# Kernel optimization log

Hardware: AMD Instinct MI355X
Metric: run time of the kernel (lower is better)

Reference implementation:

```python
import jax, jax.numpy as jnp
import numpy as np

S, B, DIN, DBERT, H, L = 128, 32, 256, 768, 512, 2
NT_POS, NT_MORPH = 32, 64


def setup_inputs() -> dict:
    key = jax.random.key(0)
    ks = iter(jax.random.split(key, 32))
    def rn(shape, s=0.1):
        return jax.random.normal(next(ks), shape, dtype=jnp.float32) * s
    D0 = DIN + DBERT  # 1024 == 2*H, so per-layer LSTM weights stack cleanly
    return {
        "src_segments": rn((S, B, DIN), 1.0),
        "bert_encodings": rn((B, DBERT), 1.0),
        "labels_pos": jax.random.randint(next(ks), (S, B), 0, NT_POS, dtype=jnp.int32),
        "labels_morph": jax.random.randint(next(ks), (S, B), 0, NT_MORPH, dtype=jnp.int32),
        # stacked LSTM params: [layer, direction, ...], PyTorch gate order i,f,g,o
        "w_ih": rn((L, 2, 4 * H, D0)),
        "w_hh": rn((L, 2, 4 * H, H)),
        "b_ih": rn((L, 2, 4 * H)),
        "b_hh": rn((L, 2, 4 * H)),
        "head_w_pos": rn((NT_POS, 2 * H)),
        "head_b_pos": rn((NT_POS,)),
        "head_w_morph": rn((NT_MORPH, 2 * H)),
        "head_b_morph": rn((NT_MORPH,)),
        "start_pos": rn((NT_POS,)), "end_pos": rn((NT_POS,)), "trans_pos": rn((NT_POS, NT_POS)),
        "start_morph": rn((NT_MORPH,)), "end_morph": rn((NT_MORPH,)), "trans_morph": rn((NT_MORPH, NT_MORPH)),
    }


def _run_dir(x, w_ih, w_hh, b):
    # x: [S, B, D]; one LSTM direction via scan over time
    bsz, hd = x.shape[1], w_hh.shape[1]
    def step(carry, xt):
        h, c = carry
        g = xt @ w_ih.T + h @ w_hh.T + b  # [B, 4H]
        i, f, gg, o = jnp.split(g, 4, axis=-1)
        c = jax.nn.sigmoid(f) * c + jax.nn.sigmoid(i) * jnp.tanh(gg)
        h = jax.nn.sigmoid(o) * jnp.tanh(c)
        return (h, c), h
    init = (jnp.zeros((bsz, hd), x.dtype), jnp.zeros((bsz, hd), x.dtype))
    _, hs = jax.lax.scan(step, init, x)
    return hs


def _bilstm(x, w_ih, w_hh, b_ih, b_hh):
    out = x
    for l in range(w_ih.shape[0]):
        b = b_ih[l] + b_hh[l]
        fwd = _run_dir(out, w_ih[l, 0], w_hh[l, 0], b[0])
        bwd = _run_dir(out[::-1], w_ih[l, 1], w_hh[l, 1], b[1])[::-1]
        out = jnp.concatenate([fwd, bwd], axis=-1)  # [S, B, 2H]
    return out


def _crf_ll(em, tags, start, trans, end):
    # torchcrf log-likelihood, mask=None, reduction='sum'. em: [S,B,K], tags: [S,B]
    bsz = em.shape[1]
    first = start[tags[0]] + em[0, jnp.arange(bsz), tags[0]]
    em_sc = jnp.take_along_axis(em, tags[..., None], axis=2)[..., 0]  # [S,B]
    num = first + trans[tags[:-1], tags[1:]].sum(0) + em_sc[1:].sum(0) + end[tags[-1]]
    def step(alpha, et):  # alpha: [B,K]
        return jax.nn.logsumexp(alpha[:, :, None] + trans[None], axis=1) + et, None
    alpha, _ = jax.lax.scan(step, start[None, :] + em[0], em[1:])
    den = jax.nn.logsumexp(alpha + end[None, :], axis=1)
    return jnp.sum(num - den)


def reference(src_segments, bert_encodings, labels_pos, labels_morph,
              w_ih, w_hh, b_ih, b_hh,
              head_w_pos, head_b_pos, head_w_morph, head_b_morph,
              start_pos, end_pos, trans_pos, start_morph, end_morph, trans_morph):
    # bert encodings are repeated over seq and concatenated on features
    bert = jnp.broadcast_to(bert_encodings[None], (src_segments.shape[0],) + bert_encodings.shape)
    emb = jnp.concatenate([src_segments, bert], axis=-1)  # dropout p=0 -> identity
    out = _bilstm(emb, w_ih, w_hh, b_ih, b_hh)            # [S,B,2H]
    feat_pos = out @ head_w_pos.T + head_b_pos            # [S,B,32]
    feat_morph = out @ head_w_morph.T + head_b_morph      # [S,B,64]
    ll = (_crf_ll(feat_pos, labels_pos, start_pos, trans_pos, end_pos)
          + _crf_ll(feat_morph, labels_morph, start_morph, trans_morph, end_morph))
    return -ll  # loss = -sum_f crf_f(emissions_f, labels_f)
```

## Files before the change

### kernel.cpp

```cpp
#include <hip/hip_runtime.h>


typedef unsigned short u16;
typedef unsigned int u32;
typedef unsigned long long u64;
typedef __attribute__((ext_vector_type(8))) __bf16 bf16x8;
typedef __attribute__((ext_vector_type(4))) float floatx4;

static __device__ __forceinline__ u16 f2bf(float f) {
  u32 u = __float_as_uint(f);
  u += 0x7fffu + ((u >> 16) & 1u);
  return (u16)(u >> 16);
}
static __device__ __forceinline__ float bf2f(u32 bits) {
  return __uint_as_float(bits << 16);
}
static __device__ __forceinline__ float sigf(float x) {
  return 1.0f / (1.0f + __expf(-x));
}
static __device__ __forceinline__ float tanh_(float x) {
  return 1.0f - 2.0f / (1.0f + __expf(2.0f * x));
}
static __device__ __forceinline__ floatx4 mfma16(bf16x8 a, bf16x8 b, floatx4 c) {
  return __builtin_amdgcn_mfma_f32_16x16x32_bf16(a, b, c, 0, 0, 0);
}

__global__ __launch_bounds__(256) void prep_kernel(
    const float* __restrict__ w_ih, const float* __restrict__ w_hh,
    const float* __restrict__ b_ih, const float* __restrict__ b_hh,
    const float* __restrict__ src,  const float* __restrict__ bert,
    const float* __restrict__ hwp,  const float* __restrict__ hbp,
    const float* __restrict__ hwm,  const float* __restrict__ hbm,
    u16* __restrict__ Wsrc, u16* __restrict__ Wbert, u16* __restrict__ Wih1,
    u16* __restrict__ Whh,  u16* __restrict__ SrcBf, u16* __restrict__ BertBf,
    u16* __restrict__ Wheads, float* __restrict__ b0sum, float* __restrict__ b1sum,
    float* __restrict__ hb, float* __restrict__ dout)
{
  const int NA = 4194304;
  const int NB = 4194304;
  const int NC = 4194304;
  const int ND = 1048576;
  const int NE = 24576;
  const int NF = 98304;
  const int NG = 8192;
  const int NH = 96;
  const int TOTAL = NA + NB + NC + ND + NE + NF + NG + NH + 1;
  for (int i = blockIdx.x * 256 + threadIdx.x; i < TOTAL; i += gridDim.x * 256) {
    int x = i;
    if (x < NA) {
      int c = x & 1023, r = x >> 10;
      float v = w_ih[x];
      if (c < 256) Wsrc[r * 256 + c] = f2bf(v);
      else         Wbert[r * 768 + (c - 256)] = f2bf(v);
      continue;
    }
    x -= NA;
    if (x < NB) { Wih1[x] = f2bf(w_ih[NA + x]); continue; }
    x -= NB;
    if (x < NC) { Whh[x] = f2bf(w_hh[x]); continue; }
    x -= NC;
    if (x < ND) { SrcBf[x] = f2bf(src[x]); continue; }
    x -= ND;
    if (x < NE) { BertBf[x] = f2bf(bert[x]); continue; }
    x -= NE;
    if (x < NF) {
      Wheads[x] = f2bf(x < 32768 ? hwp[x] : hwm[x - 32768]);
      continue;
    }
    x -= NF;
    if (x < NG) {
      float v = b_ih[x] + b_hh[x];
      if (x < 4096) b0sum[x] = v; else b1sum[x - 4096] = v;
      continue;
    }
    x -= NG;
    if (x < NH) { hb[x] = (x < 32) ? hbp[x] : hbm[x - 32]; continue; }
    dout[0] = 0.f;
  }
}

__global__ __launch_bounds__(256) void gemm_nt(
    const u16* __restrict__ A, int lda,
    const u16* __restrict__ B, int ldb,
    float* __restrict__ C, int ldc,
    int M, int N, int K,
    const float* __restrict__ bias_n,
    const float* __restrict__ auxBN, int auxld,
    int mode)
{
  __shared__ __align__(16) u16 As[128 * 64];
  __shared__ __align__(16) u16 Bs[128 * 64];
  const int m0 = blockIdx.y * 128, n0 = blockIdx.x * 128;
  const int tid = threadIdx.x;
  const int wv = tid >> 6, ln = tid & 63;
  const int wm = wv & 1, wn = wv >> 1;
  const int q = ln >> 4, l15 = ln & 15;
  floatx4 acc[4][4];
#pragma unroll
  for (int a = 0; a < 4; ++a)
#pragma unroll
    for (int b2 = 0; b2 < 4; ++b2) acc[a][b2] = (floatx4){0.f, 0.f, 0.f, 0.f};

  for (int kk = 0; kk < K; kk += 64) {
    __syncthreads();
#pragma unroll
    for (int j = 0; j < 4; ++j) {
      const int idx = j * 256 + tid;
      const int r = idx >> 3, cc = idx & 7;
      const int slot = cc ^ (r & 7);
      const int ra = min(m0 + r, M - 1);
      *(int4*)&As[r * 64 + slot * 8] = *(const int4*)&A[(long)ra * lda + kk + cc * 8];
      const int rb = min(n0 + r, N - 1);
      *(int4*)&Bs[r * 64 + slot * 8] = *(const int4*)&B[(long)rb * ldb + kk + cc * 8];
    }
    __syncthreads();
#pragma unroll
    for (int ks = 0; ks < 2; ++ks) {
      bf16x8 af[4], bf[4];
#pragma unroll
      for (int im = 0; im < 4; ++im) {
        const int r = wm * 64 + im * 16 + l15;
        const int slot = (ks * 4 + q) ^ (r & 7);
        af[im] = *(const bf16x8*)&As[r * 64 + slot * 8];
      }
#pragma unroll
      for (int jn = 0; jn < 4; ++jn) {
        const int r = wn * 64 + jn * 16 + l15;
        const int slot = (ks * 4 + q) ^ (r & 7);
        bf[jn] = *(const bf16x8*)&Bs[r * 64 + slot * 8];
      }
#pragma unroll
      for (int im = 0; im < 4; ++im)
#pragma unroll
        for (int jn = 0; jn < 4; ++jn)
          acc[im][jn] = mfma16(af[im], bf[jn], acc[im][jn]);
    }
  }
  if (mode == 0) {
#pragma unroll
    for (int im = 0; im < 4; ++im)
#pragma unroll
      for (int jn = 0; jn < 4; ++jn) {
        const int n = n0 + wn * 64 + jn * 16 + l15;
        if (n < N) {
          const float badd = bias_n ? bias_n[n] : 0.f;
#pragma unroll
          for (int rg = 0; rg < 4; ++rg) {
            const int m = m0 + wm * 64 + im * 16 + q * 4 + rg;
            if (m < M) {
              float v = acc[im][jn][rg] + badd;
              if (auxBN) v += auxBN[(long)(m & 31) * auxld + n];
              C[(long)m * ldc + n] = v;
            }
          }
        }
      }
  } else {
    u64* G = (u64*)C;
#pragma unroll
    for (int im = 0; im < 4; ++im)
#pragma unroll
      for (int jn = 0; jn < 4; ++jn) {
        const int n = n0 + wn * 64 + jn * 16 + l15;
        const int dirsel = n >> 11, nn = n & 2047;
        const int gt = nn >> 9, u = nn & 511;
        const int ub = u >> 4, low = u & 15;
        const int wvl = low >> 2, jl = low & 3;
        const int l15l = gt * 4 + jl;
        const int m = m0 + wm * 64 + im * 16 + q * 4;
        const int s = m >> 5, b0 = m & 31;
        const int mh = b0 >> 4, qq = (b0 >> 2) & 3;
        const float badd = bias_n ? bias_n[n] : 0.f;
        u64 pk = 0;
#pragma unroll
        for (int rg = 0; rg < 4; ++rg) {
          float v = acc[im][jn][rg] + badd;
          if (auxBN) v += auxBN[(long)(b0 + rg) * auxld + n];
          pk |= (u64)f2bf(v) << (16 * rg);
        }
        G[(((((long)dirsel * 128 + s) * 2 + mh) * 32 + ub) * 4 + wvl) * 64
          + l15l * 4 + qq] = pk;
      }
  }
}

__global__ __launch_bounds__(256, 1) void lstm_rec(
    const u16* __restrict__ gates,
    u16* __restrict__ out,
    const u16* __restrict__ whh)
{
  __shared__ __align__(16) u16 h_lds[16 * 512];
  __shared__ float gsc[4][16][17];
  const int bid = blockIdx.x;
  const int dir = bid >> 6;
  const int mh = (bid >> 5) & 1;
  const int ub = bid & 31;
  const int u0 = ub * 16;
  const int tid = threadIdx.x;
  const int wv = tid >> 6;
  const int ln = tid & 63;
  const int q = ln >> 4, l15 = ln & 15;

  const int gate_r = (l15 >> 2) * 512 + u0 + wv * 4 + (l15 & 3);

  bf16x8 bfrag[16];
  {
    const u16* wp = whh + ((long)dir * 2048 + gate_r) * 512 + q * 8;
#pragma unroll
    for (int ks = 0; ks < 16; ++ks)
      bfrag[ks] = *(const bf16x8*)(wp + ks * 32);
  }

  float c = 0.f;
  const int b_glob = mh * 16 + l15;

  const u64* gbase = (const u64*)gates
      + ((((long)dir * 128 * 2 + mh) * 32 + ub) * 4 + wv) * 64 + l15 * 4 + q;

  u64 gcur = gbase[(long)(dir ? 127 : 0) * 16384];
  u64 gnext = 0;

  for (int t = 0; t < 128; ++t) {
    const int s = dir ? (127 - t) : t;
    if (t < 127) {
      const int sn = dir ? (126 - t) : (t + 1);
      gnext = gbase[(long)sn * 16384];
    }
    floatx4 acc = (floatx4){0.f, 0.f, 0.f, 0.f};
    if (t > 0) {
      const int sp = dir ? (s + 1) : (s - 1);
      const u64* ubp = (const u64*)(out + (((long)sp * 32 + mh * 16) * 1024 + (long)dir * 512));
      u64 v8[8];
#pragma unroll
      for (int j = 0; j < 8; ++j) {
        const int idx = j * 256 + tid;
        const int r = idx >> 7, c4 = idx & 127;
        v8[j] = __hip_atomic_load((u64*)(ubp + (long)r * 256 + c4),
                                  __ATOMIC_RELAXED, __HIP_MEMORY_SCOPE_AGENT);
      }
      while (true) {
        bool bad = false;
#pragma unroll
        for (int j = 0; j < 8; ++j) bad |= ((v8[j] & 0xffffULL) == 0xffffULL);
        if (!bad) break;
#pragma unroll
        for (int j = 0; j < 8; ++j) {
          if ((v8[j] & 0xffffULL) == 0xffffULL) {
            const int idx = j * 256 + tid;
            const int r = idx >> 7, c4 = idx & 127;
            v8[j] = __hip_atomic_load((u64*)(ubp + (long)r * 256 + c4),
                                      __ATOMIC_RELAXED, __HIP_MEMORY_SCOPE_AGENT);
          }
        }
      }
#pragma unroll
      for (int j = 0; j < 8; ++j) {
        const int idx = j * 256 + tid;
        const int r = idx >> 7, c4 = idx & 127;
        const int cc8 = c4 >> 1, hf = c4 & 1;
        *(u64*)&h_lds[r * 512 + ((cc8 ^ (r & 7)) << 3) + (hf << 2)] = v8[j];
      }
      __syncthreads();
      floatx4 acc1 = (floatx4){0.f, 0.f, 0.f, 0.f};
#pragma unroll
      for (int ks = 0; ks < 16; ks += 2) {
        const int slot0 = (ks * 4 + q) ^ (l15 & 7);
        bf16x8 a0 = *(const bf16x8*)&h_lds[l15 * 512 + slot0 * 8];
        acc = mfma16(a0, bfrag[ks], acc);
        const int slot1 = ((ks + 1) * 4 + q) ^ (l15 & 7);
        bf16x8 a1 = *(const bf16x8*)&h_lds[l15 * 512 + slot1 * 8];
        acc1 = mfma16(a1, bfrag[ks + 1], acc1);
      }
      acc += acc1;
    }
#pragma unroll
    for (int rg = 0; rg < 4; ++rg)
      gsc[wv][q * 4 + rg][l15] = acc[rg] + bf2f((u32)((gcur >> (16 * rg)) & 0xffffu));
    const float gi = gsc[wv][l15][q];
    const float gf = gsc[wv][l15][4 + q];
    const float gg = gsc[wv][l15][8 + q];
    const float go = gsc[wv][l15][12 + q];
    const float iv = sigf(gi), fv = sigf(gf), gv = tanh_(gg), ov = sigf(go);
    c = fv * c + iv * gv;
    const float h = ov * tanh_(c);
    const u32 hv = (u32)f2bf(h);
    const u32 p1 = (u32)__shfl_xor((int)hv, 16);
    const u32 lo32 = hv | (p1 << 16);
    const u64 w64 = (u64)lo32 |
                    ((u64)(u32)__shfl_xor((int)lo32, 32) << 32);
    if (q == 0)
      __hip_atomic_store(
          (u64*)&out[((long)s * 32 + b_glob) * 1024 + dir * 512 + u0 + wv * 4],
          w64, __ATOMIC_RELAXED, __HIP_MEMORY_SCOPE_AGENT);
    gcur = gnext;
  }
}

template <int K>
static __device__ void crf_body(const float* __restrict__ feat, int off,
                                const int* __restrict__ labels, int b,
                                const float* __restrict__ start,
                                const float* __restrict__ end_,
                                const float* __restrict__ trans,
                                float* __restrict__ outp,
                                float* transT, float (*alpha)[64],
                                float* red)
{
  const int tid = threadIdx.x;
  for (int i = tid; i < K * K; i += 256) {
    int kk = i / K, kp2 = i % K;
    transT[kp2 * 65 + kk] = trans[i];
  }
  if (tid < K) alpha[0][tid] = start[tid] + feat[b * 96 + off + tid];
  __syncthreads();
  constexpr int Kq = K / 4;
  const int kp = tid >> 2, k4 = tid & 3;
  const bool act = kp < K;
  int p = 0;
  for (int s = 1; s < 128; ++s) {
    float x[Kq];
    float mx = -3e38f;
    if (act) {
      const float* tr = &transT[kp * 65 + k4 * Kq];
      const float* al = &alpha[p][k4 * Kq];
#pragma unroll
      for (int i2 = 0; i2 < Kq; ++i2) { x[i2] = al[i2] + tr[i2]; mx = fmaxf(mx, x[i2]); }
    }
    mx = fmaxf(mx, __shfl_xor(mx, 1));
    mx = fmaxf(mx, __shfl_xor(mx, 2));
    float ss = 0.f;
    if (act) {
#pragma unroll
      for (int i2 = 0; i2 < Kq; ++i2) ss += __expf(x[i2] - mx);
    }
    ss += __shfl_xor(ss, 1);
    ss += __shfl_xor(ss, 2);
    if (act && k4 == 0)
      alpha[p ^ 1][kp] = mx + __logf(ss) + feat[(s * 32 + b) * 96 + off + kp];
    __syncthreads();
    p ^= 1;
  }
  if (tid < 128) {
    const int tg = labels[tid * 32 + b];
    float term = feat[(tid * 32 + b) * 96 + off + tg];
    if (tid == 0) term += start[tg];
    else          term += trans[labels[(tid - 1) * 32 + b] * K + tg];
    if (tid == 127) term += end_[tg];
    red[tid] = term;
  }
  __syncthreads();
  if (tid == 0) {
    float num = 0.f;
    for (int i = 0; i < 128; ++i) num += red[i];
    float mx = -3e38f;
    for (int k = 0; k < K; ++k) mx = fmaxf(mx, alpha[p][k] + end_[k]);
    float ss = 0.f;
    for (int k = 0; k < K; ++k) ss += __expf(alpha[p][k] + end_[k] - mx);
    const float den = mx + __logf(ss);
    atomicAdd(outp, den - num);
  }
}

__global__ __launch_bounds__(256) void crf_kernel(
    const float* __restrict__ feat,
    const int* __restrict__ labp, const int* __restrict__ labm,
    const float* __restrict__ stp, const float* __restrict__ enp, const float* __restrict__ trp,
    const float* __restrict__ stm, const float* __restrict__ enm, const float* __restrict__ trm,
    float* __restrict__ outp)
{
  __shared__ float transT[64 * 65];
  __shared__ float alpha[2][64];
  __shared__ float red[128];
  const int task = blockIdx.x >> 5, b = blockIdx.x & 31;
  if (task == 0) crf_body<32>(feat, 0,  labp, b, stp, enp, trp, outp, transT, alpha, red);
  else           crf_body<64>(feat, 32, labm, b, stm, enm, trm, outp, transT, alpha, red);
}

extern "C" void kernel_launch(void* const* d_in, const int* in_sizes, int n_in,
                              void* d_out, int out_size, void* d_ws, size_t ws_size,
                              hipStream_t stream) {
  const float* src  = (const float*)d_in[0];
  const float* bert = (const float*)d_in[1];
  const int*   labp = (const int*)d_in[2];
  const int*   labm = (const int*)d_in[3];
  const float* w_ih = (const float*)d_in[4];
  const float* w_hh = (const float*)d_in[5];
  const float* b_ih = (const float*)d_in[6];
  const float* b_hh = (const float*)d_in[7];
  const float* hwp  = (const float*)d_in[8];
  const float* hbp  = (const float*)d_in[9];
  const float* hwm  = (const float*)d_in[10];
  const float* hbm  = (const float*)d_in[11];
  const float* stp  = (const float*)d_in[12];
  const float* enp  = (const float*)d_in[13];
  const float* trp  = (const float*)d_in[14];
  const float* stm  = (const float*)d_in[15];
  const float* enm  = (const float*)d_in[16];
  const float* trm  = (const float*)d_in[17];

  char* ws = (char*)d_ws;
  u16*   Wsrc     = (u16*)(ws + 0);
  u16*   Wbert    = (u16*)(ws + 2097152);
  u16*   Wih1     = (u16*)(ws + 8388608);
  u16*   Whh      = (u16*)(ws + 16777216);
  u16*   SrcBf    = (u16*)(ws + 25165824);
  u16*   BertBf   = (u16*)(ws + 27262976);
  u16*   Wheads   = (u16*)(ws + 27312128);
  float* b0sum    = (float*)(ws + 27508736);
  float* b1sum    = (float*)(ws + 27525120);
  float* hb       = (float*)(ws + 27541504);
  float* bertpart = (float*)(ws + 27542272);
  float* feat     = (float*)(ws + 28066560);
  u16*   out0     = (u16*)(ws + 29639424);
  u16*   out1     = (u16*)(ws + 38028032);
  u16*   gates    = (u16*)(ws + 46416640);
  float* dout     = (float*)d_out;

  hipMemsetAsync(out0, 0xFF, 8388608, stream);
  hipMemsetAsync(out1, 0xFF, 8388608, stream);

  hipLaunchKernelGGL(prep_kernel, dim3(2048), dim3(256), 0, stream,
      w_ih, w_hh, b_ih, b_hh, src, bert, hwp, hbp, hwm, hbm,
      Wsrc, Wbert, Wih1, Whh, SrcBf, BertBf, Wheads, b0sum, b1sum, hb, dout);

  hipLaunchKernelGGL(gemm_nt, dim3(32, 1), dim3(256), 0, stream,
      BertBf, 768, Wbert, 768, bertpart, 4096, 32, 4096, 768,
      b0sum, (const float*)nullptr, 0, 0);

  hipLaunchKernelGGL(gemm_nt, dim3(32, 32), dim3(256), 0, stream,
      SrcBf, 256, Wsrc, 256, (float*)gates, 0, 4096, 4096, 256,
      (const float*)nullptr, bertpart, 4096, 1);

  {
    const u16* g = gates; u16* o = out0; const u16* wh = Whh;
    void* args[] = {&g, &o, &wh};
    hipLaunchCooperativeKernel(reinterpret_cast<void*>(&lstm_rec),
                               dim3(128), dim3(256), args, 0, stream);
  }

  hipLaunchKernelGGL(gemm_nt, dim3(32, 32), dim3(256), 0, stream,
      out0, 1024, Wih1, 1024, (float*)gates, 0, 4096, 4096, 1024,
      b1sum, (const float*)nullptr, 0, 1);

  {
    const u16* g = gates; u16* o = out1; const u16* wh = Whh + 2L * 2048 * 512;
    void* args[] = {&g, &o, &wh};
    hipLaunchCooperativeKernel(reinterpret_cast<void*>(&lstm_rec),
                               dim3(128), dim3(256), args, 0, stream);
  }

  hipLaunchKernelGGL(gemm_nt, dim3(1, 32), dim3(256), 0, stream,
      out1, 1024, Wheads, 1024, feat, 96, 4096, 96, 1024,
      hb, (const float*)nullptr, 0, 0);

  hipLaunchKernelGGL(crf_kernel, dim3(64), dim3(256), 0, stream,
      feat, labp, labm, stp, enp, trp, stm, enm, trm, dout);
}
```

Before: 886.4 us.

## Overlap layer-1 input GEMM and head GEMM with LSTM recurrence via spin-waiting blocks

Fuses the LSTM recurrence kernel with consumer GEMMs in one cooperative launch. Extra blocks compute the next layer's input-gate GEMM, or the emission-head GEMM, tile by tile. Each tile spin-polls on the 0xFFFF sentinel until the recurrence has written the rows it needs, and tiles are ordered from the middle timesteps outward so both directions feed them. This hides GEMM time behind the serial recurrence and removes two kernel launches, at the cost of more CUs competing with the recurrence and polling traffic. It falls back to the separate GEMM when the workspace is too small.

```diff
diff --git a/kernel.cpp b/kernel.cpp
--- a/kernel.cpp
+++ b/kernel.cpp
@@ -23,6 +23,12 @@
 }
 static __device__ __forceinline__ floatx4 mfma16(bf16x8 a, bf16x8 b, floatx4 c) {
   return __builtin_amdgcn_mfma_f32_16x16x32_bf16(a, b, c, 0, 0, 0);
+}
+static __device__ __forceinline__ u64 aload64(const u64* p) {
+  return __hip_atomic_load((u64*)p, __ATOMIC_RELAXED, __HIP_MEMORY_SCOPE_AGENT);
+}
+static __device__ __forceinline__ void astore64(u64* p, u64 v) {
+  __hip_atomic_store(p, v, __ATOMIC_RELAXED, __HIP_MEMORY_SCOPE_AGENT);
 }
 
 __global__ __launch_bounds__(256) void prep_kernel(
@@ -184,13 +190,159 @@
   }
 }
 
-__global__ __launch_bounds__(256, 1) void lstm_rec(
-    const u16* __restrict__ gates,
-    u16* __restrict__ out,
-    const u16* __restrict__ whh)
+static __device__ void gemm_tile(
+    const u16* __restrict__ A, int lda,
+    const u16* __restrict__ B, int ldb,
+    float* __restrict__ C, int ldc,
+    int m0, int n0, int M, int N, int K,
+    const float* __restrict__ bias_n,
+    int mode, int spinA, u16* smem)
 {
-  __shared__ __align__(16) u16 h_lds[16 * 512];
-  __shared__ float gsc[4][16][17];
+  u16* As = smem;
+  u16* Bs = smem + 128 * 64;
+  const int tid = threadIdx.x;
+  const int wv = tid >> 6, ln = tid & 63;
+  const int wm = wv & 1, wn = wv >> 1;
+  const int q = ln >> 4, l15 = ln & 15;
+  floatx4 acc[4][4];
+#pragma unroll
+  for (int a = 0; a < 4; ++a)
+#pragma unroll
+    for (int b2 = 0; b2 < 4; ++b2) acc[a][b2] = (floatx4){0.f, 0.f, 0.f, 0.f};
+
+  for (int kk = 0; kk < K; kk += 64) {
+    __syncthreads();
+    if (spinA) {
+      u64 va[8];
+      const int jpoll = (kk < 512) ? 7 : 0;
+      {
+        const int idx = jpoll * 256 + tid;
+        const int r = idx >> 4, cc = idx & 15;
+        const u64* p = (const u64*)&A[(long)(m0 + r) * lda + kk + cc * 4];
+        u64 v = aload64(p);
+        int tries = 0;
+        while ((v & 0xffffULL) == 0xffffULL) {
+          if (tries < 6) { __builtin_amdgcn_s_sleep(4); ++tries; }
+          else           { __builtin_amdgcn_s_sleep(32); }
+          v = aload64(p);
+        }
+        va[jpoll] = v;
+      }
+#pragma unroll
+      for (int j = 0; j < 8; ++j) {
+        if (j == jpoll) continue;
+        const int idx = j * 256 + tid;
+        const int r = idx >> 4, cc = idx & 15;
+        va[j] = aload64((const u64*)&A[(long)(m0 + r) * lda + kk + cc * 4]);
+      }
+      while (true) {
+        bool bad = false;
+#pragma unroll
+        for (int j = 0; j < 8; ++j) bad |= ((va[j] & 0xffffULL) == 0xffffULL);
+        if (!bad) break;
+        __builtin_amdgcn_s_sleep(8);
+#pragma unroll
+        for (int j = 0; j < 8; ++j)
+          if ((va[j] & 0xffffULL) == 0xffffULL) {
+            const int idx = j * 256 + tid;
+            const int r = idx >> 4, cc = idx & 15;
+            va[j] = aload64((const u64*)&A[(long)(m0 + r) * lda + kk + cc * 4]);
+          }
+      }
+#pragma unroll
+      for (int j = 0; j < 8; ++j) {
+        const int idx = j * 256 + tid;
+        const int r = idx >> 4, cc = idx & 15;
+        const int ch = cc >> 1, hf = cc & 1;
+        *(u64*)&As[r * 64 + ((ch ^ (r & 7)) << 3) + (hf << 2)] = va[j];
+      }
+    } else {
+#pragma unroll
+      for (int j = 0; j < 4; ++j) {
+        const int idx = j * 256 + tid;
+        const int r = idx >> 3, cc = idx & 7;
+        const int slot = cc ^ (r & 7);
+        const int ra = min(m0 + r, M - 1);
+        *(int4*)&As[r * 64 + slot * 8] = *(const int4*)&A[(long)ra * lda + kk + cc * 8];
+      }
+    }
+#pragma unroll
+    for (int j = 0; j < 4; ++j) {
+      const int idx = j * 256 + tid;
+      const int r = idx >> 3, cc = idx & 7;
+      const int slot = cc ^ (r & 7);
+      const int rb = min(n0 + r, N - 1);
+      *(int4*)&Bs[r * 64 + slot * 8] = *(const int4*)&B[(long)rb * ldb + kk + cc * 8];
+    }
+    __syncthreads();
+#pragma unroll
+    for (int ks = 0; ks < 2; ++ks) {
+      bf16x8 af[4], bf[4];
+#pragma unroll
+      for (int im = 0; im < 4; ++im) {
+        const int r = wm * 64 + im * 16 + l15;
+        const int slot = (ks * 4 + q) ^ (r & 7);
+        af[im] = *(const bf16x8*)&As[r * 64 + slot * 8];
+      }
+#pragma unroll
+      for (int jn = 0; jn < 4; ++jn) {
+        const int r = wn * 64 + jn * 16 + l15;
+        const int slot = (ks * 4 + q) ^ (r & 7);
+        bf[jn] = *(const bf16x8*)&Bs[r * 64 + slot * 8];
+      }
+#pragma unroll
+      for (int im = 0; im < 4; ++im)
+#pragma unroll
+        for (int jn = 0; jn < 4; ++jn)
+          acc[im][jn] = mfma16(af[im], bf[jn], acc[im][jn]);
+    }
+  }
+  if (mode == 0) {
+#pragma unroll
+    for (int im = 0; im < 4; ++im)
+#pragma unroll
+      for (int jn = 0; jn < 4; ++jn) {
+        const int n = n0 + wn * 64 + jn * 16 + l15;
+        if (n < N) {
+          const float badd = bias_n ? bias_n[n] : 0.f;
+#pragma unroll
+          for (int rg = 0; rg < 4; ++rg) {
+            const int m = m0 + wm * 64 + im * 16 + q * 4 + rg;
+            if (m < M) C[(long)m * ldc + n] = acc[im][jn][rg] + badd;
+          }
+        }
+      }
+  } else {
+    u64* G = (u64*)C;
+#pragma unroll
+    for (int im = 0; im < 4; ++im)
+#pragma unroll
+      for (int jn = 0; jn < 4; ++jn) {
+        const int n = n0 + wn * 64 + jn * 16 + l15;
+        const int dirsel = n >> 11, nn = n & 2047;
+        const int gt = nn >> 9, u = nn & 511;
+        const int ub2 = u >> 4, low = u & 15;
+        const int wvl = low >> 2, jl = low & 3;
+        const int l15l = gt * 4 + jl;
+        const int m = m0 + wm * 64 + im * 16 + q * 4;
+        const int s = m >> 5, b0 = m & 31;
+        const int mh2 = b0 >> 4, qq = (b0 >> 2) & 3;
+        const float badd = bias_n ? bias_n[n] : 0.f;
+        u64 pk = 0;
+#pragma unroll
+        for (int rg = 0; rg < 4; ++rg)
+          pk |= (u64)f2bf(acc[im][jn][rg] + badd) << (16 * rg);
+        G[(((((long)dirsel * 128 + s) * 2 + mh2) * 32 + ub2) * 4 + wvl) * 64
+          + l15l * 4 + qq] = pk;
+      }
+  }
+}
+
+static __device__ void lstm_body(const u16* __restrict__ gates,
+                                 u16* __restrict__ out,
+                                 const u16* __restrict__ whh,
+                                 u16* h_lds, float* gscf)
+{
   const int bid = blockIdx.x;
   const int dir = bid >> 6;
   const int mh = (bid >> 5) & 1;
@@ -235,8 +387,7 @@
       for (int j = 0; j < 8; ++j) {
         const int idx = j * 256 + tid;
         const int r = idx >> 7, c4 = idx & 127;
-        v8[j] = __hip_atomic_load((u64*)(ubp + (long)r * 256 + c4),
-                                  __ATOMIC_RELAXED, __HIP_MEMORY_SCOPE_AGENT);
+        v8[j] = aload64(ubp + (long)r * 256 + c4);
       }
       while (true) {
         bool bad = false;
@@ -248,8 +399,7 @@
           if ((v8[j] & 0xffffULL) == 0xffffULL) {
             const int idx = j * 256 + tid;
             const int r = idx >> 7, c4 = idx & 127;
-            v8[j] = __hip_atomic_load((u64*)(ubp + (long)r * 256 + c4),
-                                      __ATOMIC_RELAXED, __HIP_MEMORY_SCOPE_AGENT);
+            v8[j] = aload64(ubp + (long)r * 256 + c4);
           }
         }
       }
@@ -275,11 +425,12 @@
     }
 #pragma unroll
     for (int rg = 0; rg < 4; ++rg)
-      gsc[wv][q * 4 + rg][l15] = acc[rg] + bf2f((u32)((gcur >> (16 * rg)) & 0xffffu));
-    const float gi = gsc[wv][l15][q];
-    const float gf = gsc[wv][l15][4 + q];
-    const float gg = gsc[wv][l15][8 + q];
-    const float go = gsc[wv][l15][12 + q];
+      gscf[(wv * 16 + q * 4 + rg) * 17 + l15] =
+          acc[rg] + bf2f((u32)((gcur >> (16 * rg)) & 0xffffu));
+    const float gi = gscf[(wv * 16 + l15) * 17 + q];
+    const float gf = gscf[(wv * 16 + l15) * 17 + 4 + q];
+    const float gg = gscf[(wv * 16 + l15) * 17 + 8 + q];
+    const float go = gscf[(wv * 16 + l15) * 17 + 12 + q];
     const float iv = sigf(gi), fv = sigf(gf), gv = tanh_(gg), ov = sigf(go);
     c = fv * c + iv * gv;
     const float h = ov * tanh_(c);
@@ -289,10 +440,43 @@
     const u64 w64 = (u64)lo32 |
                     ((u64)(u32)__shfl_xor((int)lo32, 32) << 32);
     if (q == 0)
-      __hip_atomic_store(
-          (u64*)&out[((long)s * 32 + b_glob) * 1024 + dir * 512 + u0 + wv * 4],
-          w64, __ATOMIC_RELAXED, __HIP_MEMORY_SCOPE_AGENT);
+      astore64((u64*)&out[((long)s * 32 + b_glob) * 1024 + dir * 512 + u0 + wv * 4], w64);
     gcur = gnext;
+  }
+}
+
+__global__ __launch_bounds__(256, 1) void fused_lstm(
+    int phase,
+    const u16* __restrict__ gatesIn,
+    u16* __restrict__ gatesOut,
+    u16* __restrict__ outw,
+    const u16* __restrict__ whh,
+    const u16* __restrict__ Wih1, const float* __restrict__ b1sum,
+    const u16* __restrict__ Wheads, const float* __restrict__ hb,
+    float* __restrict__ feat)
+{
+  __shared__ __align__(16) u16 smem[16384];
+  const int bid = blockIdx.x;
+  if (bid < 128) {
+    u16* h_lds = smem;
+    float* gscf = (float*)(smem + 8192);
+    lstm_body(gatesIn, outw, whh, h_lds, gscf);
+  } else if (phase == 0) {
+    const int g = bid - 128;
+    for (int ord = 0; ord < 8; ++ord) {
+      const int t = ord * 128 + g;
+      const int k = t >> 5, cn = t & 31;
+      const int rm = (k & 1) ? (16 + (k >> 1)) : (15 - (k >> 1));
+      gemm_tile(outw, 1024, Wih1, 1024, (float*)gatesOut, 0,
+                rm * 128, cn * 128, 4096, 4096, 1024,
+                b1sum, 1, 1, smem);
+    }
+  } else if (bid < 160) {
+    const int g = bid - 128;
+    const int rm = (g & 1) ? (16 + (g >> 1)) : (15 - (g >> 1));
+    gemm_tile(outw, 1024, Wheads, 1024, feat, 96,
+              rm * 128, 0, 4096, 96, 1024,
+              hb, 0, 1, smem);
   }
 }
 
@@ -414,7 +598,11 @@
   u16*   out0     = (u16*)(ws + 29639424);
   u16*   out1     = (u16*)(ws + 38028032);
   u16*   gates    = (u16*)(ws + 46416640);
+  u16*   gates1b  = (u16*)(ws + 79971072);
   float* dout     = (float*)d_out;
+
+  const bool bigws = (ws_size >= 113525504ULL);
+  u16* g1 = bigws ? gates1b : gates;
 
   hipMemsetAsync(out0, 0xFF, 8388608, stream);
   hipMemsetAsync(out1, 0xFF, 8388608, stream);
@@ -432,26 +620,36 @@
       (const float*)nullptr, bertpart, 4096, 1);
 
   {
-    const u16* g = gates; u16* o = out0; const u16* wh = Whh;
-    void* args[] = {&g, &o, &wh};
-    hipLaunchCooperativeKernel(reinterpret_cast<void*>(&lstm_rec),
-                               dim3(128), dim3(256), args, 0, stream);
-  }
-
-  hipLaunchKernelGGL(gemm_nt, dim3(32, 32), dim3(256), 0, stream,
-      out0, 1024, Wih1, 1024, (float*)gates, 0, 4096, 4096, 1024,
-      b1sum, (const float*)nullptr, 0, 1);
-
-  {
-    const u16* g = gates; u16* o = out1; const u16* wh = Whh + 2L * 2048 * 512;
-    void* args[] = {&g, &o, &wh};
-    hipLaunchCooperativeKernel(reinterpret_cast<void*>(&lstm_rec),
-                               dim3(128), dim3(256), args, 0, stream);
-  }
-
-  hipLaunchKernelGGL(gemm_nt, dim3(1, 32), dim3(256), 0, stream,
-      out1, 1024, Wheads, 1024, feat, 96, 4096, 96, 1024,
-      hb, (const float*)nullptr, 0, 0);
+    int ph0 = 0, ph1 = 1;
+    const u16* gin0 = gates; const u16* gin1 = g1;
+    u16* gout = g1; u16* o0 = out0; u16* o1 = out1;
+    const u16* whh0 = Whh; const u16* whh1 = Whh + 2L * 2048 * 512;
+    const u16* wih1 = Wih1; const float* b1 = b1sum;
+    const u16* whd = Wheads; const float* hbp2 = hb; float* ft = feat;
+
+    const dim3 gridA(bigws ? 256 : 128);
+    void* args0[] = {&ph0, &gin0, &gout, &o0, &whh0, &wih1, &b1, &whd, &hbp2, &ft};
+    if (hipLaunchCooperativeKernel(reinterpret_cast<void*>(&fused_lstm),
+                                   gridA, dim3(256), args0, 0, stream)
+        != hipSuccess) {
+      hipLaunchKernelGGL(fused_lstm, gridA, dim3(256), 0, stream,
+          ph0, gin0, gout, o0, whh0, wih1, b1, whd, hbp2, ft);
+    }
+
+    if (!bigws) {
+      hipLaunchKernelGGL(gemm_nt, dim3(32, 32), dim3(256), 0, stream,
+          out0, 1024, Wih1, 1024, (float*)gates, 0, 4096, 4096, 1024,
+          b1sum, (const float*)nullptr, 0, 1);
+    }
+
+    void* args1[] = {&ph1, &gin1, &gout, &o1, &whh1, &wih1, &b1, &whd, &hbp2, &ft};
+    if (hipLaunchCooperativeKernel(reinterpret_cast<void*>(&fused_lstm),
+                                   dim3(160), dim3(256), args1, 0, stream)
+        != hipSuccess) {
+      hipLaunchKernelGGL(fused_lstm, dim3(160), dim3(256), 0, stream,
+          ph1, gin1, gout, o1, whh1, wih1, b1, whd, hbp2, ft);
+    }
+  }
 
   hipLaunchKernelGGL(crf_kernel, dim3(64), dim3(256), 0, stream,
       feat, labp, labm, stp, enp, trp, stm, enm, trm, dout);
```

Result: slower. 1.147 ms (+29.4%).
